# Optimization experiments

Measured on AMD Instinct MI355X. Metric: run time of the kernel, lower is better.

Reference implementation:

```python
import jax, jax.numpy as jnp
import numpy as np
import math

N = 4096
E = 131072
IN_DIM, HID, OUT = 512, 256, 64
DEPTH = 3
RATIO = 0.5


def setup_inputs() -> dict:
    key = jax.random.key(0)
    ks = jax.random.split(key, 12)

    def w(k, fi, fo):
        return jax.random.normal(k, (fi, fo), jnp.float32) * (1.0 / np.sqrt(fi).astype(np.float32))

    return {
        "x": jax.random.normal(ks[0], (N, IN_DIM), jnp.float32),
        "edge_index": jax.random.randint(ks[1], (2, E), 0, N, jnp.int32),
        "dW0": w(ks[2], IN_DIM, HID), "dW1": w(ks[3], HID, HID),
        "dW2": w(ks[4], HID, HID), "dW3": w(ks[5], HID, HID),
        "db0": jnp.zeros((HID,), jnp.float32), "db1": jnp.zeros((HID,), jnp.float32),
        "db2": jnp.zeros((HID,), jnp.float32), "db3": jnp.zeros((HID,), jnp.float32),
        "pw0": jax.random.normal(ks[6], (HID,), jnp.float32),
        "pw1": jax.random.normal(ks[7], (HID,), jnp.float32),
        "pw2": jax.random.normal(ks[8], (HID,), jnp.float32),
        "uW0": w(ks[9], HID, HID), "uW1": w(ks[10], HID, HID), "uW2": w(ks[11], HID, OUT),
        "ub0": jnp.zeros((HID,), jnp.float32), "ub1": jnp.zeros((HID,), jnp.float32),
        "ub2": jnp.zeros((OUT,), jnp.float32),
    }


def gcn_conv(x, A, W, b):
    # GCNConv(improved=True): A_hat = A + 2I, sym-normalized.
    n = A.shape[0]
    eye = jnp.eye(n, dtype=A.dtype)
    Ah = A + 2.0 * eye
    d = Ah.sum(axis=1)
    dinv = jnp.where(d > 0, jax.lax.rsqrt(d), 0.0)
    An = dinv[:, None] * Ah * dinv[None, :]
    return An @ (x @ W) + b


def augment_adj(A):
    # add self loops, square the (weighted) adjacency, remove self loops
    n = A.shape[0]
    eye = jnp.eye(n, dtype=A.dtype)
    Al = A + eye
    A2 = Al @ Al
    return A2 * (1.0 - eye)


def topk_pool(x, A, w, k):
    # TopKPooling: score = tanh(x.w/||w||); keep top-k; gate kept features by score.
    score = jnp.tanh((x @ w) / jnp.linalg.norm(w))
    _, perm = jax.lax.top_k(score, k)
    xp = x[perm] * score[perm][:, None]
    return xp, A[perm][:, perm], perm


def _forward(x, edge_index, down_Ws, down_bs, pool_ws, up_Ws, up_bs):
    A = jnp.zeros((N, N), jnp.float32).at[edge_index[0], edge_index[1]].set(1.0)
    x = jax.nn.relu(gcn_conv(x, A, down_Ws[0], down_bs[0]))
    xs, As, perms = [x], [A], []
    n = N
    for i in range(1, DEPTH + 1):
        A = augment_adj(A)
        k = int(math.ceil(RATIO * n)); n = k
        x, A, perm = topk_pool(x, A, pool_ws[i - 1], k)
        x = jax.nn.relu(gcn_conv(x, A, down_Ws[i], down_bs[i]))
        if i < DEPTH:
            xs.append(x); As.append(A)
        perms.append(perm)
    for i in range(DEPTH):
        j = DEPTH - 1 - i
        res, A, perm = xs[j], As[j], perms[j]
        up = jnp.zeros_like(res).at[perm].set(x)   # unpool (sum_res=True)
        x = res + up
        x = gcn_conv(x, A, up_Ws[i], up_bs[i])
        if i < DEPTH - 1:
            x = jax.nn.relu(x)
    return x


def reference(x, edge_index, dW0, dW1, dW2, dW3, db0, db1, db2, db3,
              pw0, pw1, pw2, uW0, uW1, uW2, ub0, ub1, ub2):
    return _forward(x, edge_index,
                    [dW0, dW1, dW2, dW3], [db0, db1, db2, db3],
                    [pw0, pw1, pw2],
                    [uW0, uW1, uW2], [ub0, ub1, ub2])
```

## Files before the change

kernel.cpp:

```cpp
#include <hip/hip_runtime.h>
#include <math.h>

#define NN 4096
#define EE 131072
#define IN_DIM 512
#define HID 256
#define OUT_DIM 64
#define ECAP 128

typedef __attribute__((ext_vector_type(8))) short bf8_t;
typedef __attribute__((ext_vector_type(4))) float f4_t;
typedef __attribute__((ext_vector_type(8))) unsigned short us8_t;
typedef __attribute__((ext_vector_type(4))) unsigned short us4_t;

#define GAS __attribute__((address_space(1)))
#define LAS __attribute__((address_space(3)))

__device__ __forceinline__ unsigned short f2bf(float v){
  union { float f; unsigned u; } x; x.f = v;
  unsigned r = x.u + 0x7fffu + ((x.u >> 16) & 1u);
  return (unsigned short)(r >> 16);
}
__device__ __forceinline__ float bf2f(unsigned short h){
  union { float f; unsigned u; } x; x.u = ((unsigned)h) << 16;
  return x.f;
}

__device__ __forceinline__ float waveReduceSum(float v){
#pragma unroll
  for (int off = 32; off > 0; off >>= 1) v += __shfl_down(v, off);
  return v;
}

__global__ __launch_bounds__(256) void k_prep(
    const float* __restrict__ x_in, const float* __restrict__ dW0,
    const float* __restrict__ dW1, const float* __restrict__ dW2,
    const float* __restrict__ dW3, const float* __restrict__ uW0,
    const float* __restrict__ uW1, const float* __restrict__ uW2,
    unsigned* __restrict__ bits,
    unsigned short* __restrict__ xinh, unsigned short* __restrict__ xinl,
    unsigned short* __restrict__ W0th, unsigned short* __restrict__ W0tl,
    unsigned short* __restrict__ W5th, unsigned short* __restrict__ W5tl,
    unsigned short* __restrict__ W2th, unsigned short* __restrict__ W2tl)
{
  int b = blockIdx.x;
  if (b < 128){
    int base = b * 4096 + threadIdx.x;
#pragma unroll
    for (int i = 0; i < 16; ++i) bits[base + i * 256] = 0;
    return;
  }
  b -= 128;
  if (b < 2048){
    int i0 = b * 1024 + threadIdx.x;
#pragma unroll
    for (int i = 0; i < 4; ++i){
      int idx = i0 + i * 256;
      float v = x_in[idx];
      unsigned short h = f2bf(v);
      xinh[idx] = h; xinl[idx] = f2bf(v - bf2f(h));
    }
    return;
  }
  b -= 2048;
  const float* X; unsigned short *Th, *Tl; int R, C, tile;
  if (b < 128){ X = dW0; Th = W0th; Tl = W0tl; R = 512; C = 256; tile = b; }
  else if (b < 448){
    int t2 = b - 128; int z = t2 >> 6; int rem = t2 & 63;
    const float* ws[5] = {dW1, dW2, dW3, uW0, uW1};
    X = ws[z]; Th = W5th + (size_t)z * 65536; Tl = W5tl + (size_t)z * 65536;
    R = 256; C = 256; tile = rem;
  } else { X = uW2; Th = W2th; Tl = W2tl; R = 256; C = 64; tile = b - 448; }
  int tpr = C >> 5;
  int bx = (tile % tpr) * 32, by = (tile / tpr) * 32;
  __shared__ float t[32][33];
  int tx = threadIdx.x & 31, ty = threadIdx.x >> 5;
#pragma unroll
  for (int i = 0; i < 4; ++i)
    t[ty + i * 8][tx] = X[(size_t)(by + ty + i * 8) * C + bx + tx];
  __syncthreads();
#pragma unroll
  for (int i = 0; i < 4; ++i){
    float v = t[tx][ty + i * 8];
    unsigned short h = f2bf(v);
    size_t o = (size_t)(bx + ty + i * 8) * R + by + tx;
    Th[o] = h; Tl[o] = f2bf(v - bf2f(h));
  }
}

__global__ void k_build_bits(const int* __restrict__ ei, unsigned* __restrict__ bits){
  int e = blockIdx.x * blockDim.x + threadIdx.x;
  if (e < EE){
    int r = ei[e], c = ei[EE + e];
    atomicOr(&bits[r * 128 + (c >> 5)], 1u << (c & 31));
  }
}

__global__ __launch_bounds__(128) void k_ell(const unsigned* __restrict__ bits,
                                             int* __restrict__ ell, int* __restrict__ cnt,
                                             float* __restrict__ dinv){
  int r = blockIdx.x, t = threadIdx.x;
  unsigned w = bits[r * 128 + t];
  int c = __popc(w);
  __shared__ int sc[128];
  sc[t] = c; __syncthreads();
  for (int off = 1; off < 128; off <<= 1){
    int a = sc[t], b = (t >= off) ? sc[t - off] : 0;
    __syncthreads(); sc[t] = a + b; __syncthreads();
  }
  int total = sc[127];
  int pos = sc[t] - c;
  int base = r * ECAP;
  while (w){
    int b = __ffs(w) - 1; w &= w - 1;
    if (pos < ECAP) ell[base + pos] = t * 32 + b;
    pos++;
  }
  if (t == 0){
    cnt[r] = (total < ECAP) ? total : ECAP;
    dinv[r] = 1.0f / sqrtf((float)total + 2.0f);
  }
}

template<int NCOLS, int RELU, int SC>
__global__ __launch_bounds__(256) void k_spmm_ell(
    const int* __restrict__ ell, const int* __restrict__ cnt,
    const float* __restrict__ Zs, const float* __restrict__ dinv,
    const float* __restrict__ bias, float* __restrict__ out,
    const float* __restrict__ scw, float* __restrict__ score)
{
  int r = blockIdx.x;
  __shared__ int s_idx[ECAP];
  __shared__ int s_n;
  __shared__ float sh[4 * NCOLS];
  __shared__ float sd[4], sq[4];
  if (threadIdx.x == 0) s_n = cnt[r];
  for (int i = threadIdx.x; i < ECAP; i += 256) s_idx[i] = ell[r * ECAP + i];
  __syncthreads();
  int n = s_n; if (n > ECAP) n = ECAP;
  int wv = threadIdx.x >> 6, lane = threadIdx.x & 63;
  if (NCOLS == 256){
    f4_t acc = (f4_t){0.f, 0.f, 0.f, 0.f};
    for (int e = wv; e < n; e += 4){
      const f4_t* row = (const f4_t*)(Zs + (size_t)s_idx[e] * 256);
      acc += row[lane];
    }
    ((f4_t*)(sh + wv * 256))[lane] = acc;
  } else {
    float acc = 0.f;
    for (int e = wv; e < n; e += 4)
      acc += Zs[(size_t)s_idx[e] * 64 + lane];
    sh[wv * 64 + lane] = acc;
  }
  __syncthreads();
  int t = threadIdx.x;
  float o = 0.f;
  if (t < NCOLS){
    float y = sh[t] + sh[NCOLS + t] + sh[2 * NCOLS + t] + sh[3 * NCOLS + t];
    float z = Zs[(size_t)r * NCOLS + t];
    o = dinv[r] * (y + 2.0f * z) + bias[t];
    if (RELU) o = fmaxf(o, 0.f);
    out[(size_t)r * NCOLS + t] = o;
  }
  if (SC){
    float w = scw[t];
    float d = waveReduceSum(o * w);
    float q = waveReduceSum(w * w);
    if (!lane){ sd[wv] = d; sq[wv] = q; }
    __syncthreads();
    if (!t) score[r] = tanhf((sd[0] + sd[1] + sd[2] + sd[3]) / sqrtf(sq[0] + sq[1] + sq[2] + sq[3]));
  }
}

__global__ __launch_bounds__(256) void k_pool_build(
    const float* __restrict__ x0, const float* __restrict__ score,
    const int* __restrict__ perm1, const int* __restrict__ inv1,
    const int* __restrict__ ell, const int* __restrict__ cnt,
    unsigned short* __restrict__ xph, unsigned short* __restrict__ xpl,
    unsigned char* __restrict__ Rb,
    unsigned short* __restrict__ xu1h, unsigned short* __restrict__ xu1l)
{
  int b = blockIdx.x;
  if (b < 2048){
    int pr = perm1[b]; float s = score[pr];
    int c = threadIdx.x;
    float v = x0[(size_t)pr * 256 + c] * s;
    unsigned short h = f2bf(v);
    xph[(size_t)b * 256 + c] = h;
    xpl[(size_t)b * 256 + c] = f2bf(v - bf2f(h));
    return;
  }
  if (b < 6144){
    int k = b - 2048;
    __shared__ unsigned char row[2048];
    for (int i = threadIdx.x; i < 512; i += 256) ((int*)row)[i] = 0;
    __syncthreads();
    int n = cnt[k];
    for (int e = threadIdx.x; e < n; e += 256){
      int s = inv1[ell[k * ECAP + e]];
      if (s >= 0) row[s] = 1;
    }
    __syncthreads();
    if (threadIdx.x == 0){
      int sk = inv1[k];
      if (sk >= 0) row[sk] += 1;
    }
    __syncthreads();
    *(uint2*)(Rb + (size_t)k * 2048 + threadIdx.x * 8) = *(uint2*)(row + threadIdx.x * 8);
    return;
  }
  int r = b - 6144;
  if (inv1[r] < 0){
    int c = threadIdx.x;
    float v = x0[(size_t)r * 256 + c];
    unsigned short h = f2bf(v);
    xu1h[(size_t)r * 256 + c] = h;
    xu1l[(size_t)r * 256 + c] = f2bf(v - bf2f(h));
  }
}

template<int SRCL, int OUTL>
__global__ __launch_bounds__(256) void k_pp(
    const float* __restrict__ x, const float* __restrict__ score,
    const int* __restrict__ perm, const int* __restrict__ inv, int n, int k,
    unsigned short* __restrict__ xph, unsigned short* __restrict__ xpl,
    unsigned short* __restrict__ xuh, unsigned short* __restrict__ xul,
    const unsigned short* __restrict__ Ah, const unsigned short* __restrict__ Al,
    unsigned short* __restrict__ Lh, unsigned short* __restrict__ Ll,
    unsigned short* __restrict__ Rh, unsigned short* __restrict__ Rl)
{
  __shared__ float t[32][33];
  __shared__ int sinv[32];
  int b = blockIdx.x, c = threadIdx.x;
  if (b < k){
    int pr = perm[b]; float s = score[pr];
    float v = x[(size_t)pr * 256 + c] * s;
    unsigned short h = f2bf(v);
    xph[(size_t)b * 256 + c] = h;
    xpl[(size_t)b * 256 + c] = f2bf(v - bf2f(h));
    return;
  }
  b -= k;
  if (b < n){
    if (inv[b] < 0){
      float v = x[(size_t)b * 256 + c];
      unsigned short h = f2bf(v);
      xuh[(size_t)b * 256 + c] = h;
      xul[(size_t)b * 256 + c] = f2bf(v - bf2f(h));
    }
    return;
  }
  b -= n;
  if (b < k){
    int r = b, pr = perm[r];
    for (int cc = threadIdx.x; cc < n; cc += 256){
      float v = bf2f(Ah[(size_t)pr * n + cc]);
      if (SRCL) v += bf2f(Al[(size_t)pr * n + cc]);
      if (pr == cc) v += 1.f;
      unsigned short h = f2bf(v);
      Lh[(size_t)r * n + cc] = h;
      if (OUTL) Ll[(size_t)r * n + cc] = f2bf(v - bf2f(h));
    }
    return;
  }
  b -= k;
  int tpr = n >> 5;
  int kt = b / tpr, ct = b - kt * tpr;
  int tx = threadIdx.x & 31, ty = threadIdx.x >> 5;
  if (threadIdx.x < 32) sinv[threadIdx.x] = inv[ct * 32 + threadIdx.x];
#pragma unroll
  for (int i = 0; i < 4; ++i){
    int kl = ty + i * 8;
    size_t src = (size_t)(kt * 32 + kl) * n + ct * 32 + tx;
    float v = bf2f(Ah[src]);
    if (SRCL) v += bf2f(Al[src]);
    t[kl][tx] = v;
  }
  __syncthreads();
#pragma unroll
  for (int i = 0; i < 4; ++i){
    int cl = ty + i * 8;
    int s = sinv[cl];
    if (s >= 0){
      float v = t[tx][cl];
      if (kt * 32 + tx == ct * 32 + cl) v += 1.f;
      unsigned short h = f2bf(v);
      size_t o = (size_t)s * n + kt * 32 + tx;
      Rh[o] = h;
      if (OUTL) Rl[o] = f2bf(v - bf2f(h));
    }
  }
}

__global__ __launch_bounds__(256) void k_sq1(const int* __restrict__ ell, const int* __restrict__ cnt,
                                             const int* __restrict__ perm,
                                             const unsigned char* __restrict__ Rb,
                                             unsigned short* __restrict__ A1h,
                                             float* __restrict__ dinv1){
  int r = blockIdx.x;
  int pr = perm[r];
  __shared__ int s_idx[ECAP];
  __shared__ int s_n;
  __shared__ float sred[4];
  if (threadIdx.x == 0) s_n = cnt[pr];
  for (int i = threadIdx.x; i < ECAP; i += 256) s_idx[i] = ell[pr * ECAP + i];
  __syncthreads();
  int n = s_n; if (n > ECAP) n = ECAP;
  int colb = threadIdx.x * 8;
  uint2 acc = *(const uint2*)(Rb + (size_t)pr * 2048 + colb);
  for (int e = 0; e < n; ++e){
    uint2 v = *(const uint2*)(Rb + (size_t)s_idx[e] * 2048 + colb);
    acc.x += v.x; acc.y += v.y;
  }
  float fs = 0.f;
  us8_t o;
#pragma unroll
  for (int j = 0; j < 8; ++j){
    unsigned byte = ((j < 4 ? acc.x : acc.y) >> (8 * (j & 3))) & 0xFFu;
    if (colb + j == r) byte = 0;
    float f = (float)byte;
    fs += f;
    o[j] = f2bf(f);
  }
  *(us8_t*)(A1h + (size_t)r * 2048 + colb) = o;
  fs = waveReduceSum(fs);
  int lane = threadIdx.x & 63, wd = threadIdx.x >> 6;
  if (!lane) sred[wd] = fs;
  __syncthreads();
  if (!threadIdx.x)
    dinv1[r] = 1.0f / sqrtf(sred[0] + sred[1] + sred[2] + sred[3] + 2.0f);
}

template<int HAS_AL, int HAS_BL, int HAS_LL, int EPI>
__global__ __launch_bounds__(256) void k_mm(
    const unsigned short* __restrict__ Ah, const unsigned short* __restrict__ Al,
    const unsigned short* __restrict__ Bh, const unsigned short* __restrict__ Bl,
    int M, int N, int K, int KS, float* __restrict__ P,
    float* __restrict__ Cf, unsigned short* __restrict__ Ch, unsigned short* __restrict__ Cl,
    const float* __restrict__ dinv)
{
  constexpr int NARR = 2 + HAS_AL + HAS_BL;
  constexpr int BUF = NARR * 8192;
  __shared__ int4 ldsq[NARR * 512 * 2];
  char* ldsc = (char*)ldsq;

  const int tid = threadIdx.x, lane = tid & 63, wid = tid >> 6;
  const int wm = wid >> 1, wn = wid & 1;
  const int bm = blockIdx.y << 6, bn = blockIdx.x << 6;
  const int z = blockIdx.z;
  const int l15 = lane & 15, l4 = lane >> 4;

  f4_t acc[2][2];
#pragma unroll
  for (int i = 0; i < 2; ++i)
#pragma unroll
    for (int j = 0; j < 2; ++j) acc[i][j] = (f4_t){0.f, 0.f, 0.f, 0.f};

  const size_t rb = (size_t)K * 2;
  const size_t kz = (size_t)z * KS * 2;
  const char* pAh = (const char*)Ah + (size_t)bm * rb;
  const char* pAl = HAS_AL ? (const char*)Al + (size_t)bm * rb : nullptr;
  const char* pBh = (const char*)Bh + (size_t)bn * rb;
  const char* pBl = HAS_BL ? (const char*)Bl + (size_t)bn * rb : nullptr;

  auto stage = [&](int t, int b2){
    char* ldsb = ldsc + b2 * BUF;
    const size_t kb = kz + (size_t)t * 128;
#pragma unroll
    for (int it = 0; it < 2; ++it){
      const int idx = tid + (it << 8);
      const int row = idx >> 3;
      const int kc = ((idx & 7) << 4) ^ ((row & 7) << 4);
      const size_t go = (size_t)row * rb + kb + kc;
      const int lo = idx * 16;
      __builtin_amdgcn_global_load_lds((const GAS void*)(pAh + go), (LAS void*)(ldsb + lo), 16, 0, 0);
      __builtin_amdgcn_global_load_lds((const GAS void*)(pBh + go), (LAS void*)(ldsb + 8192 + lo), 16, 0, 0);
      if (HAS_AL)
        __builtin_amdgcn_global_load_lds((const GAS void*)(pAl + go), (LAS void*)(ldsb + 16384 + lo), 16, 0, 0);
      if (HAS_BL)
        __builtin_amdgcn_global_load_lds((const GAS void*)(pBl + go), (LAS void*)(ldsb + (2 + HAS_AL) * 8192 + lo), 16, 0, 0);
    }
  };

  const int T = KS >> 6;
  stage(0, 0);
  int b = 0;
  for (int t = 0; t < T; ++t){
    if (t + 1 < T){
      stage(t + 1, b ^ 1);
      if constexpr (NARR == 2) asm volatile("s_waitcnt vmcnt(4)" ::: "memory");
      else if constexpr (NARR == 3) asm volatile("s_waitcnt vmcnt(6)" ::: "memory");
      else asm volatile("s_waitcnt vmcnt(8)" ::: "memory");
    } else {
      asm volatile("s_waitcnt vmcnt(0)" ::: "memory");
    }
    __syncthreads();
    const char* ldsb = ldsc + b * BUF;
#pragma unroll
    for (int ks = 0; ks < 2; ++ks){
      bf8_t aH[2], aL[2], bH[2], bL[2];
#pragma unroll
      for (int f = 0; f < 2; ++f){
        int ar = wm * 32 + f * 16 + l15;
        int aoff = ar * 128 + (((ks * 64) + (l4 << 4)) ^ ((ar & 7) << 4));
        aH[f] = *(const bf8_t*)(ldsb + aoff);
        if (HAS_AL) aL[f] = *(const bf8_t*)(ldsb + 16384 + aoff);
        int br = wn * 32 + f * 16 + l15;
        int boff = br * 128 + (((ks * 64) + (l4 << 4)) ^ ((br & 7) << 4));
        bH[f] = *(const bf8_t*)(ldsb + 8192 + boff);
        if (HAS_BL) bL[f] = *(const bf8_t*)(ldsb + (2 + HAS_AL) * 8192 + boff);
      }
#pragma unroll
      for (int i = 0; i < 2; ++i)
#pragma unroll
        for (int j = 0; j < 2; ++j){
          acc[i][j] = __builtin_amdgcn_mfma_f32_16x16x32_bf16(aH[i], bH[j], acc[i][j], 0, 0, 0);
          if (HAS_BL) acc[i][j] = __builtin_amdgcn_mfma_f32_16x16x32_bf16(aH[i], bL[j], acc[i][j], 0, 0, 0);
          if (HAS_AL) acc[i][j] = __builtin_amdgcn_mfma_f32_16x16x32_bf16(aL[i], bH[j], acc[i][j], 0, 0, 0);
          if (HAS_LL) acc[i][j] = __builtin_amdgcn_mfma_f32_16x16x32_bf16(aL[i], bL[j], acc[i][j], 0, 0, 0);
        }
    }
    __syncthreads();
    b ^= 1;
  }

  float* Pz = (EPI == 0) ? P + (size_t)z * M * N : nullptr;
#pragma unroll
  for (int i = 0; i < 2; ++i)
#pragma unroll
    for (int j = 0; j < 2; ++j)
#pragma unroll
      for (int r = 0; r < 4; ++r){
        int grow = bm + wm * 32 + i * 16 + l4 * 4 + r;
        int gcol = bn + wn * 32 + j * 16 + l15;
        float v = acc[i][j][r];
        size_t o = (size_t)grow * N + gcol;
        if (EPI == 0){
          Pz[o] = v;
        } else if (EPI == 2){
          Cf[o] = dinv[grow] * v;
        } else {
          float sv = dinv[grow] * v;
          Cf[o] = sv;
          unsigned short h = f2bf(sv);
          size_t ot = (size_t)gcol * M + grow;
          Ch[ot] = h; Cl[ot] = f2bf(sv - bf2f(h));
        }
      }
}

template<int EPI, int SC>
__global__ __launch_bounds__(256) void k_red(
    const float* __restrict__ P, int Z, int M, int NC,
    const float* __restrict__ dinv, const float* __restrict__ Zs,
    const float* __restrict__ bias,
    float* __restrict__ Of, unsigned short* __restrict__ Oh, unsigned short* __restrict__ Ol,
    float* __restrict__ dout, int relu,
    const float* __restrict__ scw, float* __restrict__ score,
    const float* __restrict__ res, const int* __restrict__ permsel)
{
  int w = threadIdx.x >> 6, lane = threadIdx.x & 63;
  int row = blockIdx.x * 4 + w;
  int prow = (EPI == 4) ? permsel[row] : 0;
  float di = (EPI != 3) ? dinv[row] : 0.f;
  float rsum = 0.f, o_d = 0.f, o_q = 0.f;
  for (int c0 = lane * 4; c0 < NC; c0 += 256){
    size_t o = (size_t)row * NC + c0;
    f4_t s = *(const f4_t*)(P + o);
    for (int zz = 1; zz < Z; ++zz) s += *(const f4_t*)(P + (size_t)zz * M * NC + o);
    if (EPI == 2){
      f4_t z4 = *(const f4_t*)(Zs + o);
      f4_t b4 = *(const f4_t*)(bias + c0);
      f4_t out;
#pragma unroll
      for (int j = 0; j < 4; ++j){
        float v = di * (s[j] + 2.0f * z4[j]) + b4[j];
        if (relu) v = fmaxf(v, 0.f);
        out[j] = v;
      }
      *(f4_t*)(Of + o) = out;
      if (SC){
        f4_t w4 = *(const f4_t*)(scw + c0);
#pragma unroll
        for (int j = 0; j < 4; ++j){ o_d += out[j] * w4[j]; o_q += w4[j] * w4[j]; }
      }
    } else if (EPI == 3){
      us4_t h4, l4v;
#pragma unroll
      for (int j = 0; j < 4; ++j){
        float v = (c0 + j == row) ? 0.f : s[j];
        unsigned short h = f2bf(v);
        h4[j] = h; l4v[j] = f2bf(v - bf2f(h));
        rsum += v;
      }
      *(us4_t*)(Oh + o) = h4;
      *(us4_t*)(Ol + o) = l4v;
    } else {
      f4_t z4 = *(const f4_t*)(Zs + o);
      f4_t b4 = *(const f4_t*)(bias + c0);
      f4_t r4 = *(const f4_t*)(res + (size_t)prow * NC + c0);
      us4_t h4, l4v;
#pragma unroll
      for (int j = 0; j < 4; ++j){
        float v = di * (s[j] + 2.0f * z4[j]) + b4[j];
        if (relu) v = fmaxf(v, 0.f);
        float comb = r4[j] + v;
        unsigned short h = f2bf(comb);
        h4[j] = h; l4v[j] = f2bf(comb - bf2f(h));
      }
      size_t od = (size_t)prow * NC + c0;
      *(us4_t*)(Oh + od) = h4;
      *(us4_t*)(Ol + od) = l4v;
    }
  }
  if (EPI == 3){
    rsum = waveReduceSum(rsum);
    if (!lane) dout[row] = 1.0f / sqrtf(rsum + 2.0f);
  }
  if (SC){
    o_d = waveReduceSum(o_d);
    o_q = waveReduceSum(o_q);
    if (!lane) score[row] = tanhf(o_d / sqrtf(o_q));
  }
}

__global__ void k_topk(const float* __restrict__ score, int n, int k,
                       int* __restrict__ perm, int* __restrict__ inv){
  int i = blockIdx.x; float si = score[i];
  int cnt = 0;
  for (int j = threadIdx.x; j < n; j += 256){
    float sj = score[j];
    if (sj > si || (sj == si && j < i)) cnt++;
  }
#pragma unroll
  for (int off = 32; off > 0; off >>= 1) cnt += __shfl_down(cnt, off);
  __shared__ int sh[4];
  int lane = threadIdx.x & 63, wid = threadIdx.x >> 6;
  if (lane == 0) sh[wid] = cnt;
  __syncthreads();
  if (threadIdx.x == 0){
    int rank = sh[0] + sh[1] + sh[2] + sh[3];
    if (rank < k){ perm[rank] = i; inv[i] = rank; }
    else inv[i] = -1;
  }
}

extern "C" void kernel_launch(void* const* d_in, const int* in_sizes, int n_in,
                              void* d_out, int out_size, void* d_ws, size_t ws_size,
                              hipStream_t stream){
  (void)in_sizes; (void)n_in; (void)out_size;
  const float* x_in = (const float*)d_in[0];
  const int*   ei   = (const int*)d_in[1];
  const float* dW0 = (const float*)d_in[2];
  const float* dW1 = (const float*)d_in[3];
  const float* dW2 = (const float*)d_in[4];
  const float* dW3 = (const float*)d_in[5];
  const float* db0 = (const float*)d_in[6];
  const float* db1 = (const float*)d_in[7];
  const float* db2 = (const float*)d_in[8];
  const float* db3 = (const float*)d_in[9];
  const float* pw0 = (const float*)d_in[10];
  const float* pw1 = (const float*)d_in[11];
  const float* pw2 = (const float*)d_in[12];
  const float* uW0 = (const float*)d_in[13];
  const float* uW1 = (const float*)d_in[14];
  const float* uW2 = (const float*)d_in[15];
  const float* ub0 = (const float*)d_in[16];
  const float* ub1 = (const float*)d_in[17];
  const float* ub2 = (const float*)d_in[18];

  char* p = (char*)d_ws;
  auto alloc = [&](size_t nbytes) -> void* {
    void* q = (void*)p; p += (nbytes + 255) & ~(size_t)255; return q;
  };
  unsigned* bits = (unsigned*)alloc((size_t)4096 * 128 * 4);
  int* ell = (int*)alloc((size_t)4096 * ECAP * 4);
  int* cnt = (int*)alloc(4096 * 4);
  int* inv1 = (int*)alloc(4096 * 4);
  int* inv2 = (int*)alloc(2048 * 4);
  int* inv3 = (int*)alloc(1024 * 4);
  unsigned char* Rb = (unsigned char*)alloc((size_t)4096 * 2048);
  float* Pp = (float*)alloc((size_t)8 * 1024 * 1024);
  unsigned short* A1h = (unsigned short*)alloc((size_t)2048 * 2048 * 2);
  unsigned short* A2h = (unsigned short*)alloc((size_t)1024 * 1024 * 2);
  unsigned short* A2l = (unsigned short*)alloc((size_t)1024 * 1024 * 2);
  unsigned short* A3h = (unsigned short*)alloc((size_t)512 * 512 * 2);
  unsigned short* A3l = (unsigned short*)alloc((size_t)512 * 512 * 2);
  unsigned short* Lb2h = (unsigned short*)alloc((size_t)1024 * 2048 * 2);
  unsigned short* Rt2h = (unsigned short*)alloc((size_t)1024 * 2048 * 2);
  unsigned short* Lb3h = (unsigned short*)alloc((size_t)512 * 1024 * 2);
  unsigned short* Lb3l = (unsigned short*)alloc((size_t)512 * 1024 * 2);
  unsigned short* Rt3h = (unsigned short*)alloc((size_t)512 * 1024 * 2);
  unsigned short* Rt3l = (unsigned short*)alloc((size_t)512 * 1024 * 2);
  unsigned short* xinh = (unsigned short*)alloc((size_t)4096 * 512 * 2);
  unsigned short* xinl = (unsigned short*)alloc((size_t)4096 * 512 * 2);
  float* x0 = (float*)alloc((size_t)4096 * HID * 4);
  float* x1 = (float*)alloc((size_t)2048 * HID * 4);
  float* x2 = (float*)alloc((size_t)1024 * HID * 4);
  unsigned short* xu1h = (unsigned short*)alloc((size_t)4096 * HID * 2);
  unsigned short* xu1l = (unsigned short*)alloc((size_t)4096 * HID * 2);
  unsigned short* xu2h = (unsigned short*)alloc((size_t)2048 * HID * 2);
  unsigned short* xu2l = (unsigned short*)alloc((size_t)2048 * HID * 2);
  unsigned short* xu3h = (unsigned short*)alloc((size_t)1024 * HID * 2);
  unsigned short* xu3l = (unsigned short*)alloc((size_t)1024 * HID * 2);
  unsigned short* xph = (unsigned short*)alloc((size_t)2048 * HID * 2);
  unsigned short* xpl = (unsigned short*)alloc((size_t)2048 * HID * 2);
  unsigned short* W0th = (unsigned short*)alloc((size_t)256 * 512 * 2);
  unsigned short* W0tl = (unsigned short*)alloc((size_t)256 * 512 * 2);
  unsigned short* W5th = (unsigned short*)alloc((size_t)5 * 256 * 256 * 2);
  unsigned short* W5tl = (unsigned short*)alloc((size_t)5 * 256 * 256 * 2);
  unsigned short* W2th = (unsigned short*)alloc((size_t)64 * 256 * 2);
  unsigned short* W2tl = (unsigned short*)alloc((size_t)64 * 256 * 2);
  float* Zs  = (float*)alloc((size_t)4096 * HID * 4);
  unsigned short* ZsTh = (unsigned short*)alloc((size_t)256 * 2048 * 2);
  unsigned short* ZsTl = (unsigned short*)alloc((size_t)256 * 2048 * 2);
  float* dinv0 = (float*)alloc(4096 * 4);
  float* dinv1 = (float*)alloc(2048 * 4);
  float* dinv2 = (float*)alloc(1024 * 4);
  float* dinv3 = (float*)alloc(512 * 4);
  float* score = (float*)alloc(4096 * 4);
  int* perm1 = (int*)alloc(2048 * 4);
  int* perm2 = (int*)alloc(1024 * 4);
  int* perm3 = (int*)alloc(512 * 4);
  if ((size_t)(p - (char*)d_ws) > ws_size) return;

  k_prep<<<2640, 256, 0, stream>>>(x_in, dW0, dW1, dW2, dW3, uW0, uW1, uW2, bits,
                                   xinh, xinl, W0th, W0tl, W5th, W5tl, W2th, W2tl);
  k_build_bits<<<EE / 256, 256, 0, stream>>>(ei, bits);
  k_ell<<<4096, 128, 0, stream>>>(bits, ell, cnt, dinv0);

  { dim3 g(4, 64);
    k_mm<1,1,0,2><<<g, 256, 0, stream>>>(xinh, xinl, W0th, W0tl, 4096, HID, IN_DIM, IN_DIM,
                                         nullptr, Zs, nullptr, nullptr, dinv0); }
  k_spmm_ell<256,1,1><<<4096, 256, 0, stream>>>(ell, cnt, Zs, dinv0, db0, x0, pw0, score);

  k_topk<<<4096, 256, 0, stream>>>(score, 4096, 2048, perm1, inv1);
  k_pool_build<<<10240, 256, 0, stream>>>(x0, score, perm1, inv1, ell, cnt,
                                          xph, xpl, Rb, xu1h, xu1l);
  k_sq1<<<2048, 256, 0, stream>>>(ell, cnt, perm1, Rb, A1h, dinv1);
  { dim3 g(4, 32);
    k_mm<1,1,0,4><<<g, 256, 0, stream>>>(xph, xpl, W5th, W5tl, 2048, HID, HID, HID,
                                         nullptr, Zs, ZsTh, ZsTl, dinv1); }
  { dim3 g(4, 32, 4);
    k_mm<0,1,0,0><<<g, 256, 0, stream>>>(A1h, nullptr, ZsTh, ZsTl, 2048, HID, 2048, 512,
                                         Pp, nullptr, nullptr, nullptr, nullptr); }
  k_red<2,1><<<512, 256, 0, stream>>>(Pp, 4, 2048, 256, dinv1, Zs, db1,
                                      x1, nullptr, nullptr, nullptr, 1, pw1, score, nullptr, nullptr);

  k_topk<<<2048, 256, 0, stream>>>(score, 2048, 1024, perm2, inv2);
  k_pp<0,0><<<8192, 256, 0, stream>>>(x1, score, perm2, inv2, 2048, 1024,
                                      xph, xpl, xu2h, xu2l, A1h, nullptr,
                                      Lb2h, nullptr, Rt2h, nullptr);
  { dim3 g(16, 16, 2);
    k_mm<0,0,0,0><<<g, 256, 0, stream>>>(Lb2h, nullptr, Rt2h, nullptr, 1024, 1024, 2048, 1024,
                                         Pp, nullptr, nullptr, nullptr, nullptr); }
  k_red<3,0><<<256, 256, 0, stream>>>(Pp, 2, 1024, 1024, nullptr, nullptr, nullptr,
                                      nullptr, A2h, A2l, dinv2, 0, nullptr, nullptr, nullptr, nullptr);
  { dim3 g(4, 16);
    k_mm<1,1,0,4><<<g, 256, 0, stream>>>(xph, xpl, W5th + 65536, W5tl + 65536, 1024, HID, HID, HID,
                                         nullptr, Zs, ZsTh, ZsTl, dinv2); }
  { dim3 g(4, 16, 4);
    k_mm<1,1,0,0><<<g, 256, 0, stream>>>(A2h, A2l, ZsTh, ZsTl, 1024, HID, 1024, 256,
                                         Pp, nullptr, nullptr, nullptr, nullptr); }
  k_red<2,1><<<256, 256, 0, stream>>>(Pp, 4, 1024, 256, dinv2, Zs, db2,
                                      x2, nullptr, nullptr, nullptr, 1, pw2, score, nullptr, nullptr);

  k_topk<<<1024, 256, 0, stream>>>(score, 1024, 512, perm3, inv3);
  k_pp<1,1><<<3072, 256, 0, stream>>>(x2, score, perm3, inv3, 1024, 512,
                                      xph, xpl, xu3h, xu3l, A2h, A2l,
                                      Lb3h, Lb3l, Rt3h, Rt3l);
  { dim3 g(8, 8, 4);
    k_mm<1,1,1,0><<<g, 256, 0, stream>>>(Lb3h, Lb3l, Rt3h, Rt3l, 512, 512, 1024, 256,
                                         Pp, nullptr, nullptr, nullptr, nullptr); }
  k_red<3,0><<<128, 256, 0, stream>>>(Pp, 4, 512, 512, nullptr, nullptr, nullptr,
                                      nullptr, A3h, A3l, dinv3, 0, nullptr, nullptr, nullptr, nullptr);
  { dim3 g(4, 8);
    k_mm<1,1,0,4><<<g, 256, 0, stream>>>(xph, xpl, W5th + 2 * 65536, W5tl + 2 * 65536, 512, HID, HID, HID,
                                         nullptr, Zs, ZsTh, ZsTl, dinv3); }
  { dim3 g(4, 8, 4);
    k_mm<1,1,0,0><<<g, 256, 0, stream>>>(A3h, A3l, ZsTh, ZsTl, 512, HID, 512, 128,
                                         Pp, nullptr, nullptr, nullptr, nullptr); }
  k_red<4,0><<<128, 256, 0, stream>>>(Pp, 4, 512, 256, dinv3, Zs, db3,
                                      nullptr, xu3h, xu3l, nullptr, 1, nullptr, nullptr, x2, perm3);

  { dim3 g(4, 16);
    k_mm<1,1,0,4><<<g, 256, 0, stream>>>(xu3h, xu3l, W5th + 3 * 65536, W5tl + 3 * 65536, 1024, HID, HID, HID,
                                         nullptr, Zs, ZsTh, ZsTl, dinv2); }
  { dim3 g(4, 16, 4);
    k_mm<1,1,0,0><<<g, 256, 0, stream>>>(A2h, A2l, ZsTh, ZsTl, 1024, HID, 1024, 256,
                                         Pp, nullptr, nullptr, nullptr, nullptr); }
  k_red<4,0><<<256, 256, 0, stream>>>(Pp, 4, 1024, 256, dinv2, Zs, ub0,
                                      nullptr, xu2h, xu2l, nullptr, 1, nullptr, nullptr, x1, perm2);

  { dim3 g(4, 32);
    k_mm<1,1,0,4><<<g, 256, 0, stream>>>(xu2h, xu2l, W5th + 4 * 65536, W5tl + 4 * 65536, 2048, HID, HID, HID,
                                         nullptr, Zs, ZsTh, ZsTl, dinv1); }
  { dim3 g(4, 32, 4);
    k_mm<0,1,0,0><<<g, 256, 0, stream>>>(A1h, nullptr, ZsTh, ZsTl, 2048, HID, 2048, 512,
                                         Pp, nullptr, nullptr, nullptr, nullptr); }
  k_red<4,0><<<512, 256, 0, stream>>>(Pp, 4, 2048, 256, dinv1, Zs, ub1,
                                      nullptr, xu1h, xu1l, nullptr, 1, nullptr, nullptr, x0, perm1);

  { dim3 g(1, 64);
    k_mm<1,1,0,2><<<g, 256, 0, stream>>>(xu1h, xu1l, W2th, W2tl, 4096, OUT_DIM, HID, HID,
                                         nullptr, Zs, nullptr, nullptr, dinv0); }
  k_spmm_ell<64,0,0><<<4096, 256, 0, stream>>>(ell, cnt, Zs, dinv0, ub2, (float*)d_out, nullptr, nullptr);
}
```

Before: 232.5 us.

## Pack pooled adjacency to 2-bit, remap GEMM block order, template split-K reduce

```diff
diff --git a/kernel.cpp b/kernel.cpp
--- a/kernel.cpp
+++ b/kernel.cpp
@@ -177,7 +177,7 @@
     const int* __restrict__ perm1, const int* __restrict__ inv1,
     const int* __restrict__ ell, const int* __restrict__ cnt,
     unsigned short* __restrict__ xph, unsigned short* __restrict__ xpl,
-    unsigned char* __restrict__ Rb,
+    unsigned short* __restrict__ Rb2,
     unsigned short* __restrict__ xu1h, unsigned short* __restrict__ xu1l)
 {
   int b = blockIdx.x;
@@ -206,7 +206,10 @@
       if (sk >= 0) row[sk] += 1;
     }
     __syncthreads();
-    *(uint2*)(Rb + (size_t)k * 2048 + threadIdx.x * 8) = *(uint2*)(row + threadIdx.x * 8);
+    unsigned w = 0;
+#pragma unroll
+    for (int j = 0; j < 8; ++j) w |= ((unsigned)row[(threadIdx.x << 3) + j]) << (2 * j);
+    Rb2[k * 256 + threadIdx.x] = (unsigned short)w;
     return;
   }
   int r = b - 6144;
@@ -294,7 +297,7 @@
 
 __global__ __launch_bounds__(256) void k_sq1(const int* __restrict__ ell, const int* __restrict__ cnt,
                                              const int* __restrict__ perm,
-                                             const unsigned char* __restrict__ Rb,
+                                             const unsigned short* __restrict__ Rb2,
                                              unsigned short* __restrict__ A1h,
                                              float* __restrict__ dinv1){
   int r = blockIdx.x;
@@ -307,9 +310,15 @@
   __syncthreads();
   int n = s_n; if (n > ECAP) n = ECAP;
   int colb = threadIdx.x * 8;
-  uint2 acc = *(const uint2*)(Rb + (size_t)pr * 2048 + colb);
+  auto expand = [](unsigned x) -> uint2 {
+    uint2 e;
+    e.x = (x & 3) | (((x >> 2) & 3) << 8) | (((x >> 4) & 3) << 16) | (((x >> 6) & 3) << 24);
+    e.y = ((x >> 8) & 3) | (((x >> 10) & 3) << 8) | (((x >> 12) & 3) << 16) | (((x >> 14) & 3) << 24);
+    return e;
+  };
+  uint2 acc = expand(Rb2[pr * 256 + threadIdx.x]);
   for (int e = 0; e < n; ++e){
-    uint2 v = *(const uint2*)(Rb + (size_t)s_idx[e] * 2048 + colb);
+    uint2 v = expand(Rb2[s_idx[e] * 256 + threadIdx.x]);
     acc.x += v.x; acc.y += v.y;
   }
   float fs = 0.f;
@@ -346,8 +355,14 @@
 
   const int tid = threadIdx.x, lane = tid & 63, wid = tid >> 6;
   const int wm = wid >> 1, wn = wid & 1;
-  const int bm = blockIdx.y << 6, bn = blockIdx.x << 6;
-  const int z = blockIdx.z;
+  const int nbx = gridDim.x, nby = gridDim.y;
+  const int tot = nbx * nby * gridDim.z;
+  int id = blockIdx.x + nbx * (blockIdx.y + nby * blockIdx.z);
+  if ((tot & 7) == 0) id = (id & 7) * (tot >> 3) + (id >> 3);
+  const int sx = id % nbx; int remq = id / nbx;
+  const int sy = remq % nby;
+  const int bm = sy << 6, bn = sx << 6;
+  const int z = remq / nby;
   const int l15 = lane & 15, l4 = lane >> 4;
 
   f4_t acc[2][2];
@@ -449,9 +464,9 @@
       }
 }
 
-template<int EPI, int SC>
+template<int EPI, int SC, int Z>
 __global__ __launch_bounds__(256) void k_red(
-    const float* __restrict__ P, int Z, int M, int NC,
+    const float* __restrict__ P, int M, int NC,
     const float* __restrict__ dinv, const float* __restrict__ Zs,
     const float* __restrict__ bias,
     float* __restrict__ Of, unsigned short* __restrict__ Oh, unsigned short* __restrict__ Ol,
@@ -467,6 +482,7 @@
   for (int c0 = lane * 4; c0 < NC; c0 += 256){
     size_t o = (size_t)row * NC + c0;
     f4_t s = *(const f4_t*)(P + o);
+#pragma unroll
     for (int zz = 1; zz < Z; ++zz) s += *(const f4_t*)(P + (size_t)zz * M * NC + o);
     if (EPI == 2){
       f4_t z4 = *(const f4_t*)(Zs + o);
@@ -579,7 +595,7 @@
   int* inv1 = (int*)alloc(4096 * 4);
   int* inv2 = (int*)alloc(2048 * 4);
   int* inv3 = (int*)alloc(1024 * 4);
-  unsigned char* Rb = (unsigned char*)alloc((size_t)4096 * 2048);
+  unsigned short* Rb2 = (unsigned short*)alloc((size_t)4096 * 256 * 2);
   float* Pp = (float*)alloc((size_t)8 * 1024 * 1024);
   unsigned short* A1h = (unsigned short*)alloc((size_t)2048 * 2048 * 2);
   unsigned short* A2h = (unsigned short*)alloc((size_t)1024 * 1024 * 2);
@@ -636,16 +652,16 @@
 
   k_topk<<<4096, 256, 0, stream>>>(score, 4096, 2048, perm1, inv1);
   k_pool_build<<<10240, 256, 0, stream>>>(x0, score, perm1, inv1, ell, cnt,
-                                          xph, xpl, Rb, xu1h, xu1l);
-  k_sq1<<<2048, 256, 0, stream>>>(ell, cnt, perm1, Rb, A1h, dinv1);
+                                          xph, xpl, Rb2, xu1h, xu1l);
+  k_sq1<<<2048, 256, 0, stream>>>(ell, cnt, perm1, Rb2, A1h, dinv1);
   { dim3 g(4, 32);
     k_mm<1,1,0,4><<<g, 256, 0, stream>>>(xph, xpl, W5th, W5tl, 2048, HID, HID, HID,
                                          nullptr, Zs, ZsTh, ZsTl, dinv1); }
   { dim3 g(4, 32, 4);
     k_mm<0,1,0,0><<<g, 256, 0, stream>>>(A1h, nullptr, ZsTh, ZsTl, 2048, HID, 2048, 512,
                                          Pp, nullptr, nullptr, nullptr, nullptr); }
-  k_red<2,1><<<512, 256, 0, stream>>>(Pp, 4, 2048, 256, dinv1, Zs, db1,
-                                      x1, nullptr, nullptr, nullptr, 1, pw1, score, nullptr, nullptr);
+  k_red<2,1,4><<<512, 256, 0, stream>>>(Pp, 2048, 256, dinv1, Zs, db1,
+                                        x1, nullptr, nullptr, nullptr, 1, pw1, score, nullptr, nullptr);
 
   k_topk<<<2048, 256, 0, stream>>>(score, 2048, 1024, perm2, inv2);
   k_pp<0,0><<<8192, 256, 0, stream>>>(x1, score, perm2, inv2, 2048, 1024,
@@ -654,16 +670,16 @@
   { dim3 g(16, 16, 2);
     k_mm<0,0,0,0><<<g, 256, 0, stream>>>(Lb2h, nullptr, Rt2h, nullptr, 1024, 1024, 2048, 1024,
                                          Pp, nullptr, nullptr, nullptr, nullptr); }
-  k_red<3,0><<<256, 256, 0, stream>>>(Pp, 2, 1024, 1024, nullptr, nullptr, nullptr,
-                                      nullptr, A2h, A2l, dinv2, 0, nullptr, nullptr, nullptr, nullptr);
+  k_red<3,0,2><<<256, 256, 0, stream>>>(Pp, 1024, 1024, nullptr, nullptr, nullptr,
+                                        nullptr, A2h, A2l, dinv2, 0, nullptr, nullptr, nullptr, nullptr);
   { dim3 g(4, 16);
     k_mm<1,1,0,4><<<g, 256, 0, stream>>>(xph, xpl, W5th + 65536, W5tl + 65536, 1024, HID, HID, HID,
                                          nullptr, Zs, ZsTh, ZsTl, dinv2); }
   { dim3 g(4, 16, 4);
     k_mm<1,1,0,0><<<g, 256, 0, stream>>>(A2h, A2l, ZsTh, ZsTl, 1024, HID, 1024, 256,
                                          Pp, nullptr, nullptr, nullptr, nullptr); }
-  k_red<2,1><<<256, 256, 0, stream>>>(Pp, 4, 1024, 256, dinv2, Zs, db2,
-                                      x2, nullptr, nullptr, nullptr, 1, pw2, score, nullptr, nullptr);
+  k_red<2,1,4><<<256, 256, 0, stream>>>(Pp, 1024, 256, dinv2, Zs, db2,
+                                        x2, nullptr, nullptr, nullptr, 1, pw2, score, nullptr, nullptr);
 
   k_topk<<<1024, 256, 0, stream>>>(score, 1024, 512, perm3, inv3);
   k_pp<1,1><<<3072, 256, 0, stream>>>(x2, score, perm3, inv3, 1024, 512,
@@ -672,16 +688,16 @@
   { dim3 g(8, 8, 4);
     k_mm<1,1,1,0><<<g, 256, 0, stream>>>(Lb3h, Lb3l, Rt3h, Rt3l, 512, 512, 1024, 256,
                                          Pp, nullptr, nullptr, nullptr, nullptr); }
-  k_red<3,0><<<128, 256, 0, stream>>>(Pp, 4, 512, 512, nullptr, nullptr, nullptr,
-                                      nullptr, A3h, A3l, dinv3, 0, nullptr, nullptr, nullptr, nullptr);
+  k_red<3,0,4><<<128, 256, 0, stream>>>(Pp, 512, 512, nullptr, nullptr, nullptr,
+                                        nullptr, A3h, A3l, dinv3, 0, nullptr, nullptr, nullptr, nullptr);
   { dim3 g(4, 8);
     k_mm<1,1,0,4><<<g, 256, 0, stream>>>(xph, xpl, W5th + 2 * 65536, W5tl + 2 * 65536, 512, HID, HID, HID,
                                          nullptr, Zs, ZsTh, ZsTl, dinv3); }
   { dim3 g(4, 8, 4);
     k_mm<1,1,0,0><<<g, 256, 0, stream>>>(A3h, A3l, ZsTh, ZsTl, 512, HID, 512, 128,
                                          Pp, nullptr, nullptr, nullptr, nullptr); }
-  k_red<4,0><<<128, 256, 0, stream>>>(Pp, 4, 512, 256, dinv3, Zs, db3,
-                                      nullptr, xu3h, xu3l, nullptr, 1, nullptr, nullptr, x2, perm3);
+  k_red<4,0,4><<<128, 256, 0, stream>>>(Pp, 512, 256, dinv3, Zs, db3,
+                                        nullptr, xu3h, xu3l, nullptr, 1, nullptr, nullptr, x2, perm3);
 
   { dim3 g(4, 16);
     k_mm<1,1,0,4><<<g, 256, 0, stream>>>(xu3h, xu3l, W5th + 3 * 65536, W5tl + 3 * 65536, 1024, HID, HID, HID,
@@ -689,8 +705,8 @@
   { dim3 g(4, 16, 4);
     k_mm<1,1,0,0><<<g, 256, 0, stream>>>(A2h, A2l, ZsTh, ZsTl, 1024, HID, 1024, 256,
                                          Pp, nullptr, nullptr, nullptr, nullptr); }
-  k_red<4,0><<<256, 256, 0, stream>>>(Pp, 4, 1024, 256, dinv2, Zs, ub0,
-                                      nullptr, xu2h, xu2l, nullptr, 1, nullptr, nullptr, x1, perm2);
+  k_red<4,0,4><<<256, 256, 0, stream>>>(Pp, 1024, 256, dinv2, Zs, ub0,
+                                        nullptr, xu2h, xu2l, nullptr, 1, nullptr, nullptr, x1, perm2);
 
   { dim3 g(4, 32);
     k_mm<1,1,0,4><<<g, 256, 0, stream>>>(xu2h, xu2l, W5th + 4 * 65536, W5tl + 4 * 65536, 2048, HID, HID, HID,
@@ -698,8 +714,8 @@
   { dim3 g(4, 32, 4);
     k_mm<0,1,0,0><<<g, 256, 0, stream>>>(A1h, nullptr, ZsTh, ZsTl, 2048, HID, 2048, 512,
                                          Pp, nullptr, nullptr, nullptr, nullptr); }
-  k_red<4,0><<<512, 256, 0, stream>>>(Pp, 4, 2048, 256, dinv1, Zs, ub1,
-                                      nullptr, xu1h, xu1l, nullptr, 1, nullptr, nullptr, x0, perm1);
+  k_red<4,0,4><<<512, 256, 0, stream>>>(Pp, 2048, 256, dinv1, Zs, ub1,
+                                        nullptr, xu1h, xu1l, nullptr, 1, nullptr, nullptr, x0, perm1);
 
   { dim3 g(1, 64);
     k_mm<1,1,0,2><<<g, 256, 0, stream>>>(xu1h, xu1l, W2th, W2tl, 4096, OUT_DIM, HID, HID,
```

Result: no change. 228.2 us (-1.8%).
